# Kernel tuning notes

Measured on AMD Instinct MI355X. Metric: run time of the kernel, lower is better.

Reference implementation:

```python
import jax, jax.numpy as jnp
import numpy as np

B, IN, OUT = 4096, 1024, 1024


def setup_inputs() -> dict:
    key = jax.random.key(0)
    ks = jax.random.split(key, 11)
    xav = 1.0 / np.sqrt(IN + OUT)  # Xavier-style scale for sigmoid/tanh layers
    d = {
        "x": jax.random.normal(ks[0], (B, IN), dtype=jnp.float32),
        "h": jax.random.normal(ks[1], (B, OUT), dtype=jnp.float32),
        "c": jax.random.normal(ks[2], (B, OUT), dtype=jnp.float32),
        "w_f": jax.random.normal(ks[3], (IN + OUT, OUT), dtype=jnp.float32) * xav,
        "b_f": jnp.zeros((1, OUT), dtype=jnp.float32),
        "w_i": jax.random.normal(ks[4], (IN + OUT, OUT), dtype=jnp.float32) * xav,
        "b_i": jnp.zeros((1, OUT), dtype=jnp.float32),
        "w_c": jax.random.normal(ks[5], (IN + OUT, OUT), dtype=jnp.float32) * xav,
        "b_c": jnp.zeros((1, OUT), dtype=jnp.float32),
        "w_o": jax.random.normal(ks[6], (IN + OUT, OUT), dtype=jnp.float32) * xav,
        "b_o": jnp.zeros((1, OUT), dtype=jnp.float32),
    }
    return d


def reference(x, h, c, w_f, b_f, w_i, b_i, w_c, b_c, w_o, b_o):
    # combined input [B, IN+OUT]
    z = jnp.concatenate([x, h], axis=1)
    f = jax.nn.sigmoid(z @ w_f + b_f)      # forget gate
    i = jax.nn.sigmoid(z @ w_i + b_i)      # update (input) gate
    g = jnp.tanh(z @ w_c + b_c)            # candidate cell
    o = jax.nn.sigmoid(z @ w_o + b_o)      # output gate
    c_new = c * f + i * g
    h_new = jnp.tanh(c_new) * o
    return h_new
```

## Files before the change

kernel.cpp:

```cpp
#include <hip/hip_runtime.h>
#include <hip/hip_bf16.h>

typedef short short8 __attribute__((ext_vector_type(8)));
typedef float f32x4 __attribute__((ext_vector_type(4)));

#define NB 4096
#define KZ 2048
#define NG 1024
#define NT 64

__device__ __forceinline__ unsigned short f2bf(float f) {
  unsigned int u = __float_as_uint(f);
  u += 0x7FFFu + ((u >> 16) & 1u);
  return (unsigned short)(u >> 16);
}
__device__ __forceinline__ float bf2f(unsigned short s) {
  return __uint_as_float(((unsigned int)s) << 16);
}
__device__ __forceinline__ void gload_lds16(const void* g, void* l) {
  __builtin_amdgcn_global_load_lds(
      (__attribute__((address_space(1))) void*)g,
      (__attribute__((address_space(3))) void*)l, 16, 0, 0);
}
__device__ __forceinline__ float sigm(float x) { return 1.f / (1.f + __expf(-x)); }
__device__ __forceinline__ float tanh_fast(float x) {
  float e = __expf(-2.f * fabsf(x));
  float r = (1.f - e) / (1.f + e);
  return copysignf(r, x);
}

__global__ void zsplit_kernel(const float* __restrict__ x, const float* __restrict__ h,
                              unsigned short* __restrict__ zh) {
  int idx = blockIdx.x * 256 + threadIdx.x;
  int e = idx << 2;
  int r = e >> 11;
  int k = e & (KZ - 1);
  const float* src = (k < 1024) ? (x + ((size_t)r << 10) + k)
                                : (h + ((size_t)r << 10) + (k - 1024));
  float4 v = *reinterpret_cast<const float4*>(src);
  float vf[4] = {v.x, v.y, v.z, v.w};
  unsigned short hh[4];
#pragma unroll
  for (int j = 0; j < 4; ++j) hh[j] = f2bf(vf[j]);
  uint2 H = make_uint2((unsigned)hh[0] | ((unsigned)hh[1] << 16),
                       (unsigned)hh[2] | ((unsigned)hh[3] << 16));
  *reinterpret_cast<uint2*>(zh + e) = H;
}

__global__ void wsplit_kernel(const float* __restrict__ w0, const float* __restrict__ w1,
                              const float* __restrict__ w2, const float* __restrict__ w3,
                              unsigned short* __restrict__ wh, unsigned short* __restrict__ wl) {
  __shared__ float tile[32][33];
  int g = blockIdx.z;
  const float* w = (g == 0) ? w0 : (g == 1) ? w1 : (g == 2) ? w2 : w3;
  int k0 = blockIdx.x << 5;
  int n0 = blockIdx.y << 5;
  int t = threadIdx.x;
  int rk = t >> 3, q = t & 7;
  float4 v = *reinterpret_cast<const float4*>(w + (size_t)(k0 + rk) * NG + n0 + (q << 2));
  tile[rk][(q << 2) + 0] = v.x;
  tile[rk][(q << 2) + 1] = v.y;
  tile[rk][(q << 2) + 2] = v.z;
  tile[rk][(q << 2) + 3] = v.w;
  __syncthreads();
  int n = t >> 3, kq = t & 7;
  unsigned short hs[4], ls[4];
#pragma unroll
  for (int j = 0; j < 4; ++j) {
    float f = tile[(kq << 2) + j][n];
    unsigned short hi = f2bf(f);
    unsigned short lo = f2bf(f - bf2f(hi));
    hs[j] = hi; ls[j] = lo;
  }
  int nn = n0 + n;
  int p = ((nn >> 6) << 8) | (((nn >> 4) & 3) << 6) | (g << 4) | (nn & 15);
  size_t o = (size_t)p * KZ + k0 + (kq << 2);
  uint2 H = make_uint2((unsigned)hs[0] | ((unsigned)hs[1] << 16),
                       (unsigned)hs[2] | ((unsigned)hs[3] << 16));
  uint2 L = make_uint2((unsigned)ls[0] | ((unsigned)ls[1] << 16),
                       (unsigned)ls[2] | ((unsigned)ls[3] << 16));
  *reinterpret_cast<uint2*>(wh + o) = H;
  *reinterpret_cast<uint2*>(wl + o) = L;
}

#define MFMA(a, b, c) __builtin_amdgcn_mfma_f32_16x16x32_bf16((a), (b), (c), 0, 0, 0)

__global__ __launch_bounds__(512, 2) void lstm_gemm256_kernel(
    const unsigned short* __restrict__ zh,
    const unsigned short* __restrict__ wh, const unsigned short* __restrict__ wl,
    const float* __restrict__ c_in, const float* __restrict__ bf_,
    const float* __restrict__ bi_, const float* __restrict__ bc_,
    const float* __restrict__ bo_, float* __restrict__ out) {
  __shared__ unsigned short As[2 * 2 * 8192];
  __shared__ unsigned short Bs[2 * 2 * 8192];
  const int t = threadIdx.x;
  const int lane = t & 63;
  const int wid = t >> 6;
  const int wr = wid >> 2;
  const int wc = wid & 3;
  const int l15 = lane & 15;
  const int l4 = lane >> 4;

  const int bid = blockIdx.x;
  const int swz = ((bid & 7) << 5) + (bid >> 3);
  const int bx = swz & 15;
  const int by = swz >> 4;
  const int brow0 = by << 8;
  const int pcol0 = bx << 8;

  char* AsB = (char*)As;
  char* BsB = (char*)Bs;

  int aoff[2], boff[2];
#pragma unroll
  for (int j = 0; j < 2; ++j) {
    int row = (j << 6) + (t >> 3);
    int sl = (t & 7) ^ (row & 7);
    aoff[j] = (brow0 + row) * KZ + (sl << 3);
    boff[j] = (pcol0 + row) * KZ + (sl << 3);
  }
  const int ldsw = wid << 10;

  auto STAGE = [&](int s, int hx) {
    if (s >= NT) return;
    const int c = s & 1;
    const int seg = s >> 5;
    const int kk = (s & 31) << 6;
    if (hx < 2) {
      const int hb = hx * (128 * KZ);
      const int lb = c * 32768 + hx * 16384;
#pragma unroll
      for (int j = 0; j < 2; ++j)
        gload_lds16(zh + aoff[j] + hb + kk, AsB + lb + (j << 13) + ldsw);
    } else {
      const unsigned short* src = seg ? wl : wh;
      const int hb = (hx - 2) * (128 * KZ);
      const int lb = c * 32768 + (hx - 2) * 16384;
#pragma unroll
      for (int j = 0; j < 2; ++j)
        gload_lds16(src + boff[j] + hb + kk, BsB + lb + (j << 13) + ldsw);
    }
  };

  f32x4 acc[8][4];
#pragma unroll
  for (int m = 0; m < 8; ++m)
#pragma unroll
    for (int n = 0; n < 4; ++n) acc[m][n] = (f32x4){0.f, 0.f, 0.f, 0.f};

  const int rx = l15 & 7;
  const int sx0 = (l4 ^ rx) << 4;
  const int sx1 = ((4 + l4) ^ rx) << 4;
  const int aB = l15 << 7;
  const int bB = ((wc & 1) << 13) + (l15 << 7);
  const int aW = wr << 14;
  const int bW = (wc >> 1) << 14;

  short8 a0[8], a1[8], b0[4], b1[4];

  STAGE(0, 0); STAGE(0, 1); STAGE(0, 2); STAGE(0, 3);
  STAGE(1, 0);
  asm volatile("s_waitcnt vmcnt(2)" ::: "memory");
  asm volatile("s_barrier" ::: "memory");
#pragma unroll
  for (int m = 0; m < 8; ++m)
    a0[m] = *reinterpret_cast<const short8*>(AsB + aW + aB + (m << 11) + sx0);
  b0[0] = *reinterpret_cast<const short8*>(BsB + bW + bB + (0 << 11) + sx0);
  b0[1] = *reinterpret_cast<const short8*>(BsB + bW + bB + (1 << 11) + sx0);

  for (int kt = 0; kt < NT; ++kt) {
    const int c = kt & 1;
    const int abase = c * 32768 + aW;
    const int bbase = c * 32768 + bW;
    const int anext = (c ^ 1) * 32768 + aW;
    const int bnext = (c ^ 1) * 32768 + bW;

    STAGE(kt + 1, 2);
    STAGE(kt + 1, 3);
    b0[2] = *reinterpret_cast<const short8*>(BsB + bbase + bB + (2 << 11) + sx0);
    b0[3] = *reinterpret_cast<const short8*>(BsB + bbase + bB + (3 << 11) + sx0);
#pragma unroll
    for (int m = 0; m < 8; ++m)
      a1[m] = *reinterpret_cast<const short8*>(AsB + abase + aB + (m << 11) + sx1);
    b1[0] = *reinterpret_cast<const short8*>(BsB + bbase + bB + (0 << 11) + sx1);
    b1[1] = *reinterpret_cast<const short8*>(BsB + bbase + bB + (1 << 11) + sx1);
    __builtin_amdgcn_s_setprio(1);
#pragma unroll
    for (int m = 0; m < 8; ++m) {
      acc[m][0] = MFMA(a0[m], b0[0], acc[m][0]);
      acc[m][1] = MFMA(a0[m], b0[1], acc[m][1]);
    }
    __builtin_amdgcn_s_setprio(0);

    STAGE(kt + 1, 1);
    b1[2] = *reinterpret_cast<const short8*>(BsB + bbase + bB + (2 << 11) + sx1);
    b1[3] = *reinterpret_cast<const short8*>(BsB + bbase + bB + (3 << 11) + sx1);
    __builtin_amdgcn_s_setprio(1);
#pragma unroll
    for (int m = 0; m < 8; ++m) {
      acc[m][2] = MFMA(a0[m], b0[2], acc[m][2]);
      acc[m][3] = MFMA(a0[m], b0[3], acc[m][3]);
    }
    __builtin_amdgcn_s_setprio(0);

    __builtin_amdgcn_s_setprio(1);
#pragma unroll
    for (int m = 0; m < 8; ++m) {
      acc[m][0] = MFMA(a1[m], b1[0], acc[m][0]);
      acc[m][1] = MFMA(a1[m], b1[1], acc[m][1]);
    }
    __builtin_amdgcn_s_setprio(0);
    asm volatile("s_barrier" ::: "memory");

    STAGE(kt + 2, 0);
    __builtin_amdgcn_s_setprio(1);
#pragma unroll
    for (int m = 0; m < 8; ++m) {
      acc[m][2] = MFMA(a1[m], b1[2], acc[m][2]);
      acc[m][3] = MFMA(a1[m], b1[3], acc[m][3]);
    }
    __builtin_amdgcn_s_setprio(0);
    if (kt < NT - 2) {
      asm volatile("s_waitcnt vmcnt(2)" ::: "memory");
    } else {
      asm volatile("s_waitcnt vmcnt(0)" ::: "memory");
    }
    asm volatile("s_barrier" ::: "memory");
    if (kt < NT - 1) {
#pragma unroll
      for (int m = 0; m < 8; ++m)
        a0[m] = *reinterpret_cast<const short8*>(AsB + anext + aB + (m << 11) + sx0);
      b0[0] = *reinterpret_cast<const short8*>(BsB + bnext + bB + (0 << 11) + sx0);
      b0[1] = *reinterpret_cast<const short8*>(BsB + bnext + bB + (1 << 11) + sx0);
    }
  }

  const int ng = (bx << 6) + (wc << 4) + l15;
  const float vbf = bf_[ng], vbi = bi_[ng], vbc = bc_[ng], vbo = bo_[ng];
#pragma unroll
  for (int m = 0; m < 8; ++m) {
#pragma unroll
    for (int r = 0; r < 4; ++r) {
      const int row = brow0 + (wr << 7) + (m << 4) + (l4 << 2) + r;
      const float fp = acc[m][0][r] + vbf;
      const float ip = acc[m][1][r] + vbi;
      const float gp = acc[m][2][r] + vbc;
      const float op = acc[m][3][r] + vbo;
      const float co = c_in[(size_t)row * NG + ng];
      const float cnew = co * sigm(fp) + sigm(ip) * tanh_fast(gp);
      out[(size_t)row * NG + ng] = tanh_fast(cnew) * sigm(op);
    }
  }
}

extern "C" void kernel_launch(void* const* d_in, const int* in_sizes, int n_in,
                              void* d_out, int out_size, void* d_ws, size_t ws_size,
                              hipStream_t stream) {
  const float* x   = (const float*)d_in[0];
  const float* h   = (const float*)d_in[1];
  const float* c   = (const float*)d_in[2];
  const float* w_f = (const float*)d_in[3];
  const float* b_f = (const float*)d_in[4];
  const float* w_i = (const float*)d_in[5];
  const float* b_i = (const float*)d_in[6];
  const float* w_c = (const float*)d_in[7];
  const float* b_c = (const float*)d_in[8];
  const float* w_o = (const float*)d_in[9];
  const float* b_o = (const float*)d_in[10];
  float* out = (float*)d_out;

  unsigned short* zh = (unsigned short*)d_ws;
  unsigned short* wh = zh + (size_t)NB * KZ;
  unsigned short* wl = wh + (size_t)KZ * 4096;

  zsplit_kernel<<<(NB * KZ / 4) / 256, 256, 0, stream>>>(x, h, zh);
  wsplit_kernel<<<dim3(KZ / 32, NG / 32, 4), 256, 0, stream>>>(w_f, w_i, w_c, w_o, wh, wl);
  lstm_gemm256_kernel<<<256, 512, 0, stream>>>(zh, wh, wl, c,
                                               b_f, b_i, b_c, b_o, out);
}
```

Baseline: 155.5 us.

## Reuse each A tile across hi and lo weight halves in one K pass

The K loop now runs 32 steps instead of 64. Each step loads the activation tile once and multiplies it against both the high and the low bf16 weight splits, where before the A tiles were streamed twice, once per weight half. The schedule is rebuilt as eight barrier-separated phases that interleave LDS reads, staged global loads and MFMA groups. The aim is to cut A traffic and the number of loop iterations, at the cost of many more barriers and a single-buffered B tile that is overwritten mid-iteration, which carries a risk of races.

```diff
diff --git a/kernel.cpp b/kernel.cpp
--- a/kernel.cpp
+++ b/kernel.cpp
@@ -7,7 +7,7 @@
 #define NB 4096
 #define KZ 2048
 #define NG 1024
-#define NT 64
+#define NKS 32
 
 __device__ __forceinline__ unsigned short f2bf(float f) {
   unsigned int u = __float_as_uint(f);
@@ -84,6 +84,10 @@
 }
 
 #define MFMA(a, b, c) __builtin_amdgcn_mfma_f32_16x16x32_bf16((a), (b), (c), 0, 0, 0)
+#define BAR() __builtin_amdgcn_s_barrier()
+#define LGKM0() asm volatile("s_waitcnt lgkmcnt(0)" ::: "memory")
+#define PRIO1() __builtin_amdgcn_s_setprio(1)
+#define PRIO0() __builtin_amdgcn_s_setprio(0)
 
 __global__ __launch_bounds__(512, 2) void lstm_gemm256_kernel(
     const unsigned short* __restrict__ zh,
@@ -91,8 +95,9 @@
     const float* __restrict__ c_in, const float* __restrict__ bf_,
     const float* __restrict__ bi_, const float* __restrict__ bc_,
     const float* __restrict__ bo_, float* __restrict__ out) {
-  __shared__ unsigned short As[2 * 2 * 8192];
-  __shared__ unsigned short Bs[2 * 2 * 8192];
+  __shared__ unsigned short As[2 * 16384];
+  __shared__ unsigned short Bh[16384];
+  __shared__ unsigned short Bl[16384];
   const int t = threadIdx.x;
   const int lane = t & 63;
   const int wid = t >> 6;
@@ -109,7 +114,8 @@
   const int pcol0 = bx << 8;
 
   char* AsB = (char*)As;
-  char* BsB = (char*)Bs;
+  char* BhB = (char*)Bh;
+  char* BlB = (char*)Bl;
 
   int aoff[2], boff[2];
 #pragma unroll
@@ -121,24 +127,24 @@
   }
   const int ldsw = wid << 10;
 
-  auto STAGE = [&](int s, int hx) {
-    if (s >= NT) return;
-    const int c = s & 1;
-    const int seg = s >> 5;
-    const int kk = (s & 31) << 6;
+  auto STAGE = [&](int ks, int hx) {
+    if (ks >= NKS) return;
+    const int kk = ks << 6;
     if (hx < 2) {
-      const int hb = hx * (128 * KZ);
-      const int lb = c * 32768 + hx * 16384;
+      const int lb = ((ks & 1) << 15) + (hx << 14);
 #pragma unroll
       for (int j = 0; j < 2; ++j)
-        gload_lds16(zh + aoff[j] + hb + kk, AsB + lb + (j << 13) + ldsw);
+        gload_lds16(zh + aoff[j] + hx * (128 * KZ) + kk, AsB + lb + (j << 13) + ldsw);
+    } else if (hx < 4) {
+      const int h = hx - 2;
+#pragma unroll
+      for (int j = 0; j < 2; ++j)
+        gload_lds16(wh + boff[j] + h * (128 * KZ) + kk, BhB + (h << 14) + (j << 13) + ldsw);
     } else {
-      const unsigned short* src = seg ? wl : wh;
-      const int hb = (hx - 2) * (128 * KZ);
-      const int lb = c * 32768 + (hx - 2) * 16384;
+      const int h = hx - 4;
 #pragma unroll
       for (int j = 0; j < 2; ++j)
-        gload_lds16(src + boff[j] + hb + kk, BsB + lb + (j << 13) + ldsw);
+        gload_lds16(wl + boff[j] + h * (128 * KZ) + kk, BlB + (h << 14) + (j << 13) + ldsw);
     }
   };
 
@@ -156,83 +162,104 @@
   const int aW = wr << 14;
   const int bW = (wc >> 1) << 14;
 
-  short8 a0[8], a1[8], b0[4], b1[4];
-
-  STAGE(0, 0); STAGE(0, 1); STAGE(0, 2); STAGE(0, 3);
-  STAGE(1, 0);
-  asm volatile("s_waitcnt vmcnt(2)" ::: "memory");
-  asm volatile("s_barrier" ::: "memory");
-#pragma unroll
-  for (int m = 0; m < 8; ++m)
-    a0[m] = *reinterpret_cast<const short8*>(AsB + aW + aB + (m << 11) + sx0);
-  b0[0] = *reinterpret_cast<const short8*>(BsB + bW + bB + (0 << 11) + sx0);
-  b0[1] = *reinterpret_cast<const short8*>(BsB + bW + bB + (1 << 11) + sx0);
-
-  for (int kt = 0; kt < NT; ++kt) {
-    const int c = kt & 1;
-    const int abase = c * 32768 + aW;
-    const int bbase = c * 32768 + bW;
-    const int anext = (c ^ 1) * 32768 + aW;
-    const int bnext = (c ^ 1) * 32768 + bW;
-
-    STAGE(kt + 1, 2);
-    STAGE(kt + 1, 3);
-    b0[2] = *reinterpret_cast<const short8*>(BsB + bbase + bB + (2 << 11) + sx0);
-    b0[3] = *reinterpret_cast<const short8*>(BsB + bbase + bB + (3 << 11) + sx0);
-#pragma unroll
-    for (int m = 0; m < 8; ++m)
+  short8 a0[8], a1[8], bh0[4], bh1[4], bl0[4], bl1[4];
+
+  STAGE(0, 0); STAGE(0, 1); STAGE(0, 2); STAGE(0, 3); STAGE(0, 4); STAGE(0, 5);
+  asm volatile("s_waitcnt vmcnt(4)" ::: "memory");
+  BAR();
+
+  for (int ks = 0; ks < NKS; ++ks) {
+    const int abase = ((ks & 1) << 15) + aW;
+    const bool last = (ks == NKS - 1);
+
+#pragma unroll
+    for (int m = 0; m < 4; ++m)
+      a0[m] = *reinterpret_cast<const short8*>(AsB + abase + aB + (m << 11) + sx0);
+#pragma unroll
+    for (int n = 0; n < 4; ++n)
+      bh0[n] = *reinterpret_cast<const short8*>(BhB + bW + bB + (n << 11) + sx0);
+    BAR(); LGKM0(); PRIO1();
+#pragma unroll
+    for (int m = 0; m < 4; ++m)
+#pragma unroll
+      for (int n = 0; n < 4; ++n) acc[m][n] = MFMA(a0[m], bh0[n], acc[m][n]);
+    PRIO0(); BAR();
+
+#pragma unroll
+    for (int m = 4; m < 8; ++m)
+      a0[m] = *reinterpret_cast<const short8*>(AsB + abase + aB + (m << 11) + sx0);
+    BAR(); LGKM0(); PRIO1();
+#pragma unroll
+    for (int m = 0; m < 4; ++m)
+#pragma unroll
+      for (int n = 0; n < 4; ++n) acc[m + 4][n] = MFMA(a0[m + 4], bh0[n], acc[m + 4][n]);
+    PRIO0(); BAR();
+
+#pragma unroll
+    for (int m = 0; m < 4; ++m)
       a1[m] = *reinterpret_cast<const short8*>(AsB + abase + aB + (m << 11) + sx1);
-    b1[0] = *reinterpret_cast<const short8*>(BsB + bbase + bB + (0 << 11) + sx1);
-    b1[1] = *reinterpret_cast<const short8*>(BsB + bbase + bB + (1 << 11) + sx1);
-    __builtin_amdgcn_s_setprio(1);
-#pragma unroll
-    for (int m = 0; m < 8; ++m) {
-      acc[m][0] = MFMA(a0[m], b0[0], acc[m][0]);
-      acc[m][1] = MFMA(a0[m], b0[1], acc[m][1]);
-    }
-    __builtin_amdgcn_s_setprio(0);
-
-    STAGE(kt + 1, 1);
-    b1[2] = *reinterpret_cast<const short8*>(BsB + bbase + bB + (2 << 11) + sx1);
-    b1[3] = *reinterpret_cast<const short8*>(BsB + bbase + bB + (3 << 11) + sx1);
-    __builtin_amdgcn_s_setprio(1);
-#pragma unroll
-    for (int m = 0; m < 8; ++m) {
-      acc[m][2] = MFMA(a0[m], b0[2], acc[m][2]);
-      acc[m][3] = MFMA(a0[m], b0[3], acc[m][3]);
-    }
-    __builtin_amdgcn_s_setprio(0);
-
-    __builtin_amdgcn_s_setprio(1);
-#pragma unroll
-    for (int m = 0; m < 8; ++m) {
-      acc[m][0] = MFMA(a1[m], b1[0], acc[m][0]);
-      acc[m][1] = MFMA(a1[m], b1[1], acc[m][1]);
-    }
-    __builtin_amdgcn_s_setprio(0);
-    asm volatile("s_barrier" ::: "memory");
-
-    STAGE(kt + 2, 0);
-    __builtin_amdgcn_s_setprio(1);
-#pragma unroll
-    for (int m = 0; m < 8; ++m) {
-      acc[m][2] = MFMA(a1[m], b1[2], acc[m][2]);
-      acc[m][3] = MFMA(a1[m], b1[3], acc[m][3]);
-    }
-    __builtin_amdgcn_s_setprio(0);
-    if (kt < NT - 2) {
-      asm volatile("s_waitcnt vmcnt(2)" ::: "memory");
-    } else {
-      asm volatile("s_waitcnt vmcnt(0)" ::: "memory");
-    }
-    asm volatile("s_barrier" ::: "memory");
-    if (kt < NT - 1) {
-#pragma unroll
-      for (int m = 0; m < 8; ++m)
-        a0[m] = *reinterpret_cast<const short8*>(AsB + anext + aB + (m << 11) + sx0);
-      b0[0] = *reinterpret_cast<const short8*>(BsB + bnext + bB + (0 << 11) + sx0);
-      b0[1] = *reinterpret_cast<const short8*>(BsB + bnext + bB + (1 << 11) + sx0);
-    }
+#pragma unroll
+    for (int n = 0; n < 4; ++n)
+      bh1[n] = *reinterpret_cast<const short8*>(BhB + bW + bB + (n << 11) + sx1);
+    STAGE(ks + 1, 0);
+    BAR(); LGKM0(); PRIO1();
+#pragma unroll
+    for (int m = 0; m < 4; ++m)
+#pragma unroll
+      for (int n = 0; n < 4; ++n) acc[m][n] = MFMA(a1[m], bh1[n], acc[m][n]);
+    PRIO0(); BAR();
+
+#pragma unroll
+    for (int m = 4; m < 8; ++m)
+      a1[m] = *reinterpret_cast<const short8*>(AsB + abase + aB + (m << 11) + sx1);
+    STAGE(ks + 1, 1);
+    if (!last) { asm volatile("s_waitcnt vmcnt(4)" ::: "memory"); }
+    else       { asm volatile("s_waitcnt vmcnt(0)" ::: "memory"); }
+    BAR(); LGKM0(); PRIO1();
+#pragma unroll
+    for (int m = 0; m < 4; ++m)
+#pragma unroll
+      for (int n = 0; n < 4; ++n) acc[m + 4][n] = MFMA(a1[m + 4], bh1[n], acc[m + 4][n]);
+    PRIO0(); BAR();
+
+#pragma unroll
+    for (int n = 0; n < 4; ++n)
+      bl0[n] = *reinterpret_cast<const short8*>(BlB + bW + bB + (n << 11) + sx0);
+    STAGE(ks + 1, 2);
+    BAR(); LGKM0(); PRIO1();
+#pragma unroll
+    for (int m = 0; m < 4; ++m)
+#pragma unroll
+      for (int n = 0; n < 4; ++n) acc[m][n] = MFMA(a0[m], bl0[n], acc[m][n]);
+    PRIO0(); BAR();
+
+#pragma unroll
+    for (int n = 0; n < 4; ++n)
+      bl1[n] = *reinterpret_cast<const short8*>(BlB + bW + bB + (n << 11) + sx1);
+    STAGE(ks + 1, 3);
+    BAR(); LGKM0(); PRIO1();
+#pragma unroll
+    for (int m = 0; m < 4; ++m)
+#pragma unroll
+      for (int n = 0; n < 4; ++n) acc[m + 4][n] = MFMA(a0[m + 4], bl0[n], acc[m + 4][n]);
+    PRIO0(); BAR();
+
+    STAGE(ks + 1, 4);
+    BAR(); PRIO1();
+#pragma unroll
+    for (int m = 0; m < 4; ++m)
+#pragma unroll
+      for (int n = 0; n < 4; ++n) acc[m][n] = MFMA(a1[m], bl1[n], acc[m][n]);
+    PRIO0(); BAR();
+
+    STAGE(ks + 1, 5);
+    if (!last) { asm volatile("s_waitcnt vmcnt(4)" ::: "memory"); }
+    BAR(); PRIO1();
+#pragma unroll
+    for (int m = 0; m < 4; ++m)
+#pragma unroll
+      for (int n = 0; n < 4; ++n) acc[m + 4][n] = MFMA(a1[m + 4], bl1[n], acc[m + 4][n]);
+    PRIO0(); BAR();
   }
 
   const int ng = (bx << 6) + (wc << 4) + l15;
```

Result: faster. 130.5 us (-16.1%).
